# Kernel optimization log

Measured on AMD Instinct MI355X. Metric: run time of the kernel, lower is better.

Reference implementation:

```python
import jax, jax.numpy as jnp
import numpy as np

B, N, DIM = 4, 2048, 256
K = 16            # num_nearest_neighbors
EDGE_DIM = 2
M_DIM = 64
EIN = 2 * DIM + 1 + EDGE_DIM   # 515, edge_mlp input dim
VALID_RADIUS = 0.0
MASK_FILL = 1e5


def setup_inputs() -> dict:
    key = jax.random.key(0)
    ks = jax.random.split(key, 16)
    emb = jax.random.normal(ks[0], (B, N, DIM), dtype=jnp.float32)
    coors = jax.random.normal(ks[1], (B, N, 3), dtype=jnp.float32)
    adj = jax.random.bernoulli(ks[2], 0.004, (B, N, N))            # avg degree ~8
    feat = jax.random.normal(ks[3], (B, N, N, EDGE_DIM), dtype=jnp.float32)
    mask = jax.random.bernoulli(ks[4], 0.9, (B, N))
    s = 0.02
    eW1 = jax.random.normal(ks[5], (EIN, 2 * EIN), dtype=jnp.float32) * s
    eb1 = jnp.zeros((2 * EIN,), dtype=jnp.float32)
    eW2 = jax.random.normal(ks[6], (2 * EIN, M_DIM), dtype=jnp.float32) * s
    eb2 = jnp.zeros((M_DIM,), dtype=jnp.float32)
    nW1 = jax.random.normal(ks[7], (DIM + M_DIM, 2 * DIM), dtype=jnp.float32) * s
    nb1 = jnp.zeros((2 * DIM,), dtype=jnp.float32)
    nW2 = jax.random.normal(ks[8], (2 * DIM, DIM), dtype=jnp.float32) * s
    nb2 = jnp.zeros((DIM,), dtype=jnp.float32)
    return {"emb": emb, "coors": coors, "adj": adj, "feat": feat, "mask": mask,
            "eW1": eW1, "eb1": eb1, "eW2": eW2, "eb2": eb2,
            "nW1": nW1, "nb1": nb1, "nW2": nW2, "nb2": nb2}


def reference(emb, coors, adj, feat, mask, eW1, eb1, eW2, eb2, nW1, nb1, nW2, nb2):
    b, n, d = emb.shape
    # pairwise squared distances [b,n,n]
    rel = coors[:, :, None, :] - coors[:, None, :, :]
    rel_dist = jnp.sum(rel * rel, axis=-1)
    # ranking for kNN selection (masked pairs pushed far, self=-1, adjacent=0)
    rank_mask = mask[:, :, None] & mask[:, None, :]
    ranking = jnp.where(rank_mask, rel_dist, MASK_FILL)
    eye = jnp.eye(n, dtype=bool)[None]
    adj_ns = adj & ~eye
    ranking = jnp.where(eye, -1.0, ranking)
    ranking = jnp.where(adj_ns, 0.0, ranking)
    # k smallest
    neg_vals, idx = jax.lax.top_k(-ranking, K)          # idx [b,n,K]
    nbhd_ranking = -neg_vals
    nbhd_mask = nbhd_ranking <= VALID_RADIUS
    # gathers
    rel_dist_k = jnp.take_along_axis(rel_dist, idx, axis=2)[..., None]      # [b,n,K,1]
    edges_k = jnp.take_along_axis(feat, idx[..., None], axis=2)             # [b,n,K,E]
    feats_j = jax.vmap(lambda f, ix: f[ix])(emb, idx)                       # [b,n,K,d]
    feats_i = jnp.broadcast_to(emb[:, :, None, :], feats_j.shape)
    edge_input = jnp.concatenate([feats_i, feats_j, rel_dist_k, edges_k], axis=-1)
    # edge MLP: Linear -> SiLU -> Linear -> SiLU (dropout=0 in eval)
    h = jax.nn.silu(edge_input @ eW1 + eb1)
    m_ij = jax.nn.silu(h @ eW2 + eb2)                                       # [b,n,K,m]
    # pair mask
    mask_j = jax.vmap(lambda m, ix: m[ix])(mask, idx)                       # [b,n,K]
    pair_mask = (mask[:, :, None] & mask_j) & nbhd_mask
    m_ij = jnp.where(pair_mask[..., None], m_ij, 0.0)
    m_i = jnp.sum(m_ij, axis=2)                                             # [b,n,m]
    # node MLP with residual (norm_feats=False)
    node_in = jnp.concatenate([emb, m_i], axis=-1)
    node_out = jax.nn.silu(node_in @ nW1 + nb1) @ nW2 + nb2 + emb
    # update_coors=False -> coors unchanged; module returns full tuple
    return (node_out, coors, adj, feat, mask)
```

## Files before the change

### kernel.cpp

```cpp
#include <hip/hip_runtime.h>
#include <stdint.h>

typedef unsigned short ushort_t;

#define NN    2048
#define DIMC  256
#define H1    1030
#define MD    64
#define NROWS 8192

#define HP       1040

#define KPAD     1152
#define CH       288
#define CH_STEPS 9
#define NCHUNK   4
#define APAD     296
#define GPC      36

#define NPQ      2060
#define NPQP     2112
#define KN1      320
#define KN2      512

typedef __bf16 bf16x8 __attribute__((ext_vector_type(8)));
typedef float  f32x4  __attribute__((ext_vector_type(4)));
typedef float  f32x2  __attribute__((ext_vector_type(2)));
typedef ushort_t u16x8 __attribute__((ext_vector_type(8)));

__device__ __forceinline__ float bfu2f(ushort_t u){ union{unsigned u; float f;} v; v.u = ((unsigned)u)<<16; return v.f; }
__device__ __forceinline__ ushort_t f2bfu(float f){ union{float f; unsigned u;} v; v.f=f; unsigned r = (v.u + 0x7FFFu + ((v.u>>16)&1u))>>16; return (ushort_t)r; }
__device__ __forceinline__ float siluf(float x){ return x / (1.0f + __expf(-x)); }
__device__ __forceinline__ void split_hilo(float v, ushort_t& hi, ushort_t& lo){
    hi = f2bfu(v);
    lo = f2bfu(v - bfu2f(hi));
}

__global__ void mask_kernel(const int* __restrict__ mask, float* __restrict__ out_mask){
    int t = blockIdx.x*256 + threadIdx.x;
    if (t < NROWS) out_mask[t] = mask[t] ? 1.0f : 0.0f;
}

__global__ void adj_kernel(const int* __restrict__ adj, const int* __restrict__ mask,
                           float* __restrict__ out_adj, int* __restrict__ pairs,
                           int* __restrict__ counter)
{
    const int w = threadIdx.x >> 6, lane = threadIdx.x & 63;
    const int row = blockIdx.x*4 + w;
    const int b = row >> 11, i = row & (NN-1);
    __shared__ int nbrs[4][15];
    int total = 0;
    const size_t rbase = (size_t)row * NN;
    for (int c = 0; c < NN/64; c++) {
        int j = c*64 + lane;
        int v = adj[rbase + j];
        out_adj[rbase + j] = v ? 1.0f : 0.0f;
        bool pred = (v != 0) && (j != i);
        unsigned long long bm = __ballot(pred);
        if (pred) {
            int slot = total + __popcll(bm & ((1ull<<lane)-1ull));
            if (slot < 15) nbrs[w][slot] = j;
        }
        total += __popcll(bm);
    }
    int cnt = total < 15 ? total : 15;
    if (mask[row] != 0) {
        int jl = (lane < cnt) ? nbrs[w][lane] : 0;
        bool ok = (lane < cnt) && (mask[b*NN + jl] != 0);
        unsigned long long bm = __ballot(ok);
        int npair = 1 + __popcll(bm);
        int basep = 0;
        if (lane == 0) basep = atomicAdd(counter, npair);
        basep = __shfl(basep, 0);
        if (lane == 0) pairs[basep] = (row << 16) | i;
        if (ok) {
            int pos = basep + 1 + __popcll(bm & ((1ull<<lane)-1ull));
            pairs[pos] = (row << 16) | jl;
        }
    }
}

template<int K>
__device__ __forceinline__ void mfma_tile2(const ushort_t* __restrict__ Ah, const ushort_t* __restrict__ Al, int sA,
                                           const ushort_t* __restrict__ Bh, const ushort_t* __restrict__ Bl, int sB,
                                           int lane, f32x4 (&acc)[2][4])
{
    const int m16 = lane & 15, kg = lane >> 4;
    const ushort_t* a0h = Ah + (size_t)m16*sA + kg*8;
    const ushort_t* a0l = Al + (size_t)m16*sA + kg*8;
    const ushort_t* a1h = a0h + (size_t)16*sA;
    const ushort_t* a1l = a0l + (size_t)16*sA;
    const ushort_t* brh = Bh + (size_t)m16*sB + kg*8;
    const ushort_t* brl = Bl + (size_t)m16*sB + kg*8;
#pragma unroll 4
    for (int ks = 0; ks < K/32; ks++) {
        bf16x8 a0h_ = *reinterpret_cast<const bf16x8*>(a0h + ks*32);
        bf16x8 a0l_ = *reinterpret_cast<const bf16x8*>(a0l + ks*32);
        bf16x8 a1h_ = *reinterpret_cast<const bf16x8*>(a1h + ks*32);
        bf16x8 a1l_ = *reinterpret_cast<const bf16x8*>(a1l + ks*32);
#pragma unroll
        for (int nf = 0; nf < 4; nf++) {
            bf16x8 bh = *reinterpret_cast<const bf16x8*>(brh + (size_t)(nf*16)*sB + ks*32);
            bf16x8 bl = *reinterpret_cast<const bf16x8*>(brl + (size_t)(nf*16)*sB + ks*32);
            acc[0][nf] = __builtin_amdgcn_mfma_f32_16x16x32_bf16(a0h_, bh, acc[0][nf], 0, 0, 0);
            acc[0][nf] = __builtin_amdgcn_mfma_f32_16x16x32_bf16(a0h_, bl, acc[0][nf], 0, 0, 0);
            acc[0][nf] = __builtin_amdgcn_mfma_f32_16x16x32_bf16(a0l_, bh, acc[0][nf], 0, 0, 0);
            acc[1][nf] = __builtin_amdgcn_mfma_f32_16x16x32_bf16(a1h_, bh, acc[1][nf], 0, 0, 0);
            acc[1][nf] = __builtin_amdgcn_mfma_f32_16x16x32_bf16(a1h_, bl, acc[1][nf], 0, 0, 0);
            acc[1][nf] = __builtin_amdgcn_mfma_f32_16x16x32_bf16(a1l_, bh, acc[1][nf], 0, 0, 0);
        }
    }
}

__global__ void prep_emb(const float* __restrict__ emb, ushort_t* __restrict__ Ah, ushort_t* __restrict__ Al){
    int t = blockIdx.x*256 + threadIdx.x;
    if (t >= NROWS*DIMC) return;
    int r = t >> 8, k = t & 255;
    ushort_t hi, lo; split_hilo(emb[t], hi, lo);
    Ah[(size_t)r*KN1 + k] = hi; Al[(size_t)r*KN1 + k] = lo;
}

__global__ void prep_macc(const float* __restrict__ macc, ushort_t* __restrict__ Ah, ushort_t* __restrict__ Al){
    int t = blockIdx.x*256 + threadIdx.x;
    if (t >= NROWS*MD) return;
    int r = t >> 6, k = t & 63;
    ushort_t hi, lo; split_hilo(macc[t], hi, lo);
    Ah[(size_t)r*KN1 + DIMC + k] = hi; Al[(size_t)r*KN1 + DIMC + k] = lo;
}

__global__ void prep_weights(const float* __restrict__ eW1, const float* __restrict__ nW1,
                             const float* __restrict__ nW2, const float* __restrict__ eW2,
                             const float* __restrict__ eb1,
                             ushort_t* __restrict__ Wpq_h, ushort_t* __restrict__ Wpq_l,
                             ushort_t* __restrict__ W1T_h, ushort_t* __restrict__ W1T_l,
                             ushort_t* __restrict__ NW2T_h, ushort_t* __restrict__ NW2T_l,
                             ushort_t* __restrict__ W2T, float* __restrict__ wt4)
{
    int t = blockIdx.x*256 + threadIdx.x;
    if (t < NPQP*DIMC) {
        int n = t >> 8, k = t & 255;
        float v = 0.f;
        if (n < H1) v = eW1[(size_t)k*H1 + n];
        else if (n < NPQ) v = eW1[(size_t)(256+k)*H1 + (n - H1)];
        ushort_t hi, lo; split_hilo(v, hi, lo);
        Wpq_h[t] = hi; Wpq_l[t] = lo;
        return;
    }
    t -= NPQP*DIMC;
    if (t < 512*KN1) {
        int n = t / KN1, k = t - n*KN1;
        ushort_t hi, lo; split_hilo(nW1[(size_t)k*512 + n], hi, lo);
        W1T_h[t] = hi; W1T_l[t] = lo;
        return;
    }
    t -= 512*KN1;
    if (t < 256*KN2) {
        int n = t >> 9, k = t & 511;
        ushort_t hi, lo; split_hilo(nW2[(size_t)k*256 + n], hi, lo);
        NW2T_h[t] = hi; NW2T_l[t] = lo;
        return;
    }
    t -= 256*KN2;
    if (t < MD*KPAD) {
        int n = t / KPAD, k = t - n*KPAD;
        W2T[t] = f2bfu((k < H1) ? eW2[(size_t)k*MD + n] : 0.0f);
        return;
    }
    t -= MD*KPAD;
    if (t < 4*HP) {
        int c = t / HP, k = t - c*HP;
        float v = 0.f;
        if (k < H1) v = (c < 3) ? eW1[(size_t)(512+c)*H1 + k] : eb1[k];
        wt4[t] = v;
    }
}

__global__ __launch_bounds__(256)
void gemm_pq_mfma(const ushort_t* __restrict__ Aeph, const ushort_t* __restrict__ Aepl,
                  const ushort_t* __restrict__ Wh, const ushort_t* __restrict__ Wl,
                  ushort_t* __restrict__ Pb, ushort_t* __restrict__ Qb)
{
    const int lane = threadIdx.x & 63, w = threadIdx.x >> 6;
    const int rowBase = blockIdx.x*128 + w*32;
    const int colBase = blockIdx.y*64;
    f32x4 acc[2][4] = {{{0,0,0,0},{0,0,0,0},{0,0,0,0},{0,0,0,0}},
                       {{0,0,0,0},{0,0,0,0},{0,0,0,0},{0,0,0,0}}};
    mfma_tile2<DIMC>(Aeph + (size_t)rowBase*KN1, Aepl + (size_t)rowBase*KN1, KN1,
                     Wh + (size_t)colBase*DIMC, Wl + (size_t)colBase*DIMC, DIMC, lane, acc);
    const int m16 = lane & 15, kg = lane >> 4;
#pragma unroll
    for (int tt = 0; tt < 2; tt++) {
#pragma unroll
        for (int nf = 0; nf < 4; nf++) {
#pragma unroll
            for (int r = 0; r < 4; r++) {
                int row = rowBase + tt*16 + kg*4 + r;
                int n = colBase + nf*16 + m16;
                ushort_t v = f2bfu(acc[tt][nf][r]);
                if (n < H1)        Pb[(size_t)row*HP + n] = v;
                else if (n < NPQ)  Qb[(size_t)row*HP + (n - H1)] = v;
            }
        }
    }
}

__global__ __launch_bounds__(256)
void node1_mfma(const ushort_t* __restrict__ Aeph, const ushort_t* __restrict__ Aepl,
                const ushort_t* __restrict__ W1h, const ushort_t* __restrict__ W1l,
                const float* __restrict__ nb1, ushort_t* __restrict__ Hh, ushort_t* __restrict__ Hl)
{
    const int lane = threadIdx.x & 63, w = threadIdx.x >> 6;
    const int rowBase = blockIdx.x*128 + w*32;
    const int colBase = blockIdx.y*64;
    f32x4 acc[2][4] = {{{0,0,0,0},{0,0,0,0},{0,0,0,0},{0,0,0,0}},
                       {{0,0,0,0},{0,0,0,0},{0,0,0,0},{0,0,0,0}}};
    mfma_tile2<KN1>(Aeph + (size_t)rowBase*KN1, Aepl + (size_t)rowBase*KN1, KN1,
                    W1h + (size_t)colBase*KN1, W1l + (size_t)colBase*KN1, KN1, lane, acc);
    const int m16 = lane & 15, kg = lane >> 4;
#pragma unroll
    for (int tt = 0; tt < 2; tt++) {
#pragma unroll
        for (int nf = 0; nf < 4; nf++) {
#pragma unroll
            for (int r = 0; r < 4; r++) {
                int row = rowBase + tt*16 + kg*4 + r;
                int col = colBase + nf*16 + m16;
                float s = siluf(acc[tt][nf][r] + nb1[col]);
                ushort_t hi, lo; split_hilo(s, hi, lo);
                Hh[(size_t)row*KN2 + col] = hi;
                Hl[(size_t)row*KN2 + col] = lo;
            }
        }
    }
}

__global__ __launch_bounds__(256)
void node2_mfma(const ushort_t* __restrict__ Hh, const ushort_t* __restrict__ Hl,
                const ushort_t* __restrict__ W2h, const ushort_t* __restrict__ W2l,
                const float* __restrict__ nb2, const float* __restrict__ emb,
                float* __restrict__ out_node)
{
    const int lane = threadIdx.x & 63, w = threadIdx.x >> 6;
    const int rowBase = blockIdx.x*128 + w*32;
    const int colBase = blockIdx.y*64;
    f32x4 acc[2][4] = {{{0,0,0,0},{0,0,0,0},{0,0,0,0},{0,0,0,0}},
                       {{0,0,0,0},{0,0,0,0},{0,0,0,0},{0,0,0,0}}};
    mfma_tile2<KN2>(Hh + (size_t)rowBase*KN2, Hl + (size_t)rowBase*KN2, KN2,
                    W2h + (size_t)colBase*KN2, W2l + (size_t)colBase*KN2, KN2, lane, acc);
    const int m16 = lane & 15, kg = lane >> 4;
#pragma unroll
    for (int tt = 0; tt < 2; tt++) {
#pragma unroll
        for (int nf = 0; nf < 4; nf++) {
#pragma unroll
            for (int r = 0; r < 4; r++) {
                int row = rowBase + tt*16 + kg*4 + r;
                int col = colBase + nf*16 + m16;
                size_t o = (size_t)row*DIMC + col;
                out_node[o] = acc[tt][nf][r] + nb2[col] + emb[o];
            }
        }
    }
}

__global__ __launch_bounds__(256)
void edge_mfma(const int* __restrict__ pairs, const int* __restrict__ counter,
               const ushort_t* __restrict__ P, const ushort_t* __restrict__ Q,
               const float* __restrict__ coors, const float* __restrict__ feat,
               const float* __restrict__ wt4,
               const ushort_t* __restrict__ W2T, const float* __restrict__ eb2,
               float* __restrict__ macc)
{
    const int np = counter[0];
    const int base = blockIdx.x * 16;
    if (base >= np) return;

    __shared__ __align__(16) ushort_t Ahi[16][APAD];
    __shared__ __align__(16) ushort_t Alo[16][APAD];
    __shared__ int   s_row[16];
    __shared__ int   s_jr[16];
    __shared__ int   s_val[16];
    __shared__ float s_d[16], s_f0[16], s_f1[16];

    const int t = threadIdx.x;
    const int lane = t & 63;
    const int w = t >> 6;

    if (t < 16) {
        int ip = base + t;
        int valid = (ip < np) ? 1 : 0;
        int e = valid ? pairs[ip] : 0;
        int row = e >> 16, j = e & 0xFFFF;
        int jr = ((row >> 11) << 11) + j;
        float dx = coors[(size_t)row*3+0] - coors[(size_t)jr*3+0];
        float dy = coors[(size_t)row*3+1] - coors[(size_t)jr*3+1];
        float dz = coors[(size_t)row*3+2] - coors[(size_t)jr*3+2];
        size_t fo = ((size_t)row*NN + j)*2;
        s_row[t] = row; s_jr[t] = jr; s_val[t] = valid;
        s_d[t] = dx*dx + dy*dy + dz*dz;
        s_f0[t] = feat[fo]; s_f1[t] = feat[fo+1];
    }
    __syncthreads();

    const int pp  = lane >> 4;
    const int sub = lane & 15;
    const int p   = w*4 + pp;
    const int prow = s_row[p], pjr = s_jr[p];
    const float pd = s_d[p], pf0 = s_f0[p], pf1 = s_f1[p];
    const ushort_t* Prow = P + (size_t)prow*HP;
    const ushort_t* Qrow = Q + (size_t)pjr*HP;

    const float* w512 = wt4 + 0*HP;
    const float* w513 = wt4 + 1*HP;
    const float* w514 = wt4 + 2*HP;
    const float* bia1 = wt4 + 3*HP;

    f32x4 acc = {0.f, 0.f, 0.f, 0.f};

    const int m16  = lane & 15;
    const int kg   = lane >> 4;
    const int ncol = w*16 + m16;
    const ushort_t* wrowbase = W2T + (size_t)ncol * KPAD + kg*8;

    for (int chunk = 0; chunk < NCHUNK; chunk++) {
        const int c0 = chunk * CH;
#pragma unroll
        for (int it = 0; it < 3; it++) {
            int g = sub + it*16;
            if (g < GPC) {
                int cb  = g*8;
                int ccb = c0 + cb;
                u16x8 hv = {0,0,0,0,0,0,0,0};
                u16x8 lv = {0,0,0,0,0,0,0,0};
                if (ccb < H1) {
                    u16x8 pv8 = *reinterpret_cast<const u16x8*>(Prow + ccb);
                    u16x8 qv8 = *reinterpret_cast<const u16x8*>(Qrow + ccb);
                    f32x2 wa[4], wb[4], wc[4], wd[4];
#pragma unroll
                    for (int q = 0; q < 4; q++) {
                        wa[q] = *reinterpret_cast<const f32x2*>(w512 + ccb + q*2);
                        wb[q] = *reinterpret_cast<const f32x2*>(w513 + ccb + q*2);
                        wc[q] = *reinterpret_cast<const f32x2*>(w514 + ccb + q*2);
                        wd[q] = *reinterpret_cast<const f32x2*>(bia1 + ccb + q*2);
                    }
#pragma unroll
                    for (int e = 0; e < 8; e++) {
                        float x = bfu2f(pv8[e]) + bfu2f(qv8[e])
                                + pd*wa[e>>1][e&1] + pf0*wb[e>>1][e&1] + pf1*wc[e>>1][e&1] + wd[e>>1][e&1];
                        float h = (ccb + e < H1) ? siluf(x) : 0.f;
                        union {float f; unsigned u;} cv; cv.f = h;
                        unsigned hib = cv.u & 0xFFFF0000u;
                        hv[e] = (ushort_t)(hib >> 16);
                        union {unsigned u; float f;} hf; hf.u = hib;
                        union {float f; unsigned u;} lw; lw.f = h - hf.f;
                        lv[e] = (ushort_t)(lw.u >> 16);
                    }
                }
                *reinterpret_cast<u16x8*>(&Ahi[p][cb]) = hv;
                *reinterpret_cast<u16x8*>(&Alo[p][cb]) = lv;
            }
        }
        __syncthreads();
        const ushort_t* wrow = wrowbase + c0;
#pragma unroll
        for (int ks = 0; ks < CH_STEPS; ks++) {
            int k = ks*32 + kg*8;
            bf16x8 ahi = *reinterpret_cast<const bf16x8*>(&Ahi[m16][k]);
            bf16x8 alo = *reinterpret_cast<const bf16x8*>(&Alo[m16][k]);
            bf16x8 bfr = *reinterpret_cast<const bf16x8*>(wrow + ks*32);
            acc = __builtin_amdgcn_mfma_f32_16x16x32_bf16(ahi, bfr, acc, 0, 0, 0);
            acc = __builtin_amdgcn_mfma_f32_16x16x32_bf16(alo, bfr, acc, 0, 0, 0);
        }
        __syncthreads();
    }

    {
        float bias = eb2[ncol];
#pragma unroll
        for (int r = 0; r < 4; r++) {
            int pe = kg*4 + r;
            if (s_val[pe]) {
                float m = siluf(acc[r] + bias);
                atomicAdd(&macc[(size_t)s_row[pe]*MD + ncol], m);
            }
        }
    }
}

extern "C" void kernel_launch(void* const* d_in, const int* in_sizes, int n_in,
                              void* d_out, int out_size, void* d_ws, size_t ws_size,
                              hipStream_t stream)
{
    const float* emb   = (const float*)d_in[0];
    const float* coors = (const float*)d_in[1];
    const int*   adj   = (const int*)d_in[2];
    const float* feat  = (const float*)d_in[3];
    const int*   mask  = (const int*)d_in[4];
    const float* eW1   = (const float*)d_in[5];
    const float* eb1   = (const float*)d_in[6];
    const float* eW2   = (const float*)d_in[7];
    const float* eb2   = (const float*)d_in[8];
    const float* nW1   = (const float*)d_in[9];
    const float* nb1   = (const float*)d_in[10];
    const float* nW2   = (const float*)d_in[11];
    const float* nb2   = (const float*)d_in[12];

    float* out       = (float*)d_out;
    float* out_node  = out;
    float* out_coors = out + 2097152;
    float* out_adj   = out + 2121728;
    float* out_feat  = out + 18898944;
    float* out_mask  = out + 52453376;

    char* ws = (char*)d_ws;
    int*      counter = (int*)(ws + 0);
    float*    macc    = (float*)(ws + 256);
    int*      pairs   = (int*)(ws + 2097408);
    ushort_t* Pbuf    = (ushort_t*)(ws + 2621696);
    float*    wt4     = (float*)(ws + 19661056);

    char* scr = (char*)out_feat;
    ushort_t* Aep_h = (ushort_t*)(scr + 0);
    ushort_t* Aep_l = (ushort_t*)(scr + 5242880);
    ushort_t* Wpq_h = (ushort_t*)(scr + 10485760);
    ushort_t* Wpq_l = (ushort_t*)(scr + 11567104);
    ushort_t* W1T_h = (ushort_t*)(scr + 12648448);
    ushort_t* W1T_l = (ushort_t*)(scr + 12976128);
    ushort_t* NW2T_h= (ushort_t*)(scr + 13303808);
    ushort_t* NW2T_l= (ushort_t*)(scr + 13565952);
    ushort_t* Hid_h = (ushort_t*)(scr + 13828096);
    ushort_t* Hid_l = (ushort_t*)(scr + 22216704);
    ushort_t* Qbuf  = (ushort_t*)(scr + 30605312);

    ushort_t* W2T = (ushort_t*)out_node;

    hipMemsetAsync(counter, 0, 256, stream);
    hipMemsetAsync(macc, 0, (size_t)NROWS*MD*sizeof(float), stream);

    hipMemcpyAsync(out_coors, coors, (size_t)24576*sizeof(float), hipMemcpyDeviceToDevice, stream);

    mask_kernel<<<(NROWS + 255)/256, 256, 0, stream>>>(mask, out_mask);
    adj_kernel<<<NROWS/4, 256, 0, stream>>>(adj, mask, out_adj, pairs, counter);

    prep_emb<<<(NROWS*DIMC + 255)/256, 256, 0, stream>>>(emb, Aep_h, Aep_l);
    {
        int tot = NPQP*DIMC + 512*KN1 + 256*KN2 + MD*KPAD + 4*HP;
        prep_weights<<<(tot + 255)/256, 256, 0, stream>>>(eW1, nW1, nW2, eW2, eb1,
                                                          Wpq_h, Wpq_l, W1T_h, W1T_l,
                                                          NW2T_h, NW2T_l, W2T, wt4);
    }

    gemm_pq_mfma<<<dim3(NROWS/128, NPQP/64), 256, 0, stream>>>(Aep_h, Aep_l, Wpq_h, Wpq_l, Pbuf, Qbuf);

    edge_mfma<<<NROWS*16/16, 256, 0, stream>>>(pairs, counter, Pbuf, Qbuf, coors, feat,
                                               wt4, W2T, eb2, macc);

    prep_macc<<<(NROWS*MD + 255)/256, 256, 0, stream>>>(macc, Aep_h, Aep_l);
    node1_mfma<<<dim3(NROWS/128, 512/64), 256, 0, stream>>>(Aep_h, Aep_l, W1T_h, W1T_l, nb1, Hid_h, Hid_l);
    node2_mfma<<<dim3(NROWS/128, DIMC/64), 256, 0, stream>>>(Hid_h, Hid_l, NW2T_h, NW2T_l, nb2, emb, out_node);

    hipMemcpyAsync(out_feat, feat, (size_t)33554432*sizeof(float), hipMemcpyDeviceToDevice, stream);
}
```

Baseline: 770.3 us.

## Restructure edge kernel per-wave, fold bias into PQ GEMM, merge prep kernels

The edge MLP kernel now gives each wave its own 16 pairs with the hidden activations kept in registers, so the shared-memory staging and block barriers are gone and each wave computes all 64 output columns. The first-layer bias eb1 is added in the PQ GEMM epilogue instead of per edge. The mask conversion is folded into the adjacency kernel, which now reads int4 vectors, and the emb hi/lo split is merged into prep_weights. This cuts kernel launches and synchronisation, but each wave now reloads W2T rows from global memory and does more atomics per wave.

```diff
diff --git a/kernel.cpp b/kernel.cpp
--- a/kernel.cpp
+++ b/kernel.cpp
@@ -11,12 +11,8 @@
 
 #define HP       1040
 
-#define KPAD     1152
-#define CH       288
-#define CH_STEPS 9
-#define NCHUNK   4
-#define APAD     296
-#define GPC      36
+#define KPAD     1056
+#define NKS      33
 
 #define NPQ      2060
 #define NPQP     2112
@@ -25,7 +21,6 @@
 
 typedef __bf16 bf16x8 __attribute__((ext_vector_type(8)));
 typedef float  f32x4  __attribute__((ext_vector_type(4)));
-typedef float  f32x2  __attribute__((ext_vector_type(2)));
 typedef ushort_t u16x8 __attribute__((ext_vector_type(8)));
 
 __device__ __forceinline__ float bfu2f(ushort_t u){ union{unsigned u; float f;} v; v.u = ((unsigned)u)<<16; return v.f; }
@@ -36,14 +31,9 @@
     lo = f2bfu(v - bfu2f(hi));
 }
 
-__global__ void mask_kernel(const int* __restrict__ mask, float* __restrict__ out_mask){
-    int t = blockIdx.x*256 + threadIdx.x;
-    if (t < NROWS) out_mask[t] = mask[t] ? 1.0f : 0.0f;
-}
-
 __global__ void adj_kernel(const int* __restrict__ adj, const int* __restrict__ mask,
-                           float* __restrict__ out_adj, int* __restrict__ pairs,
-                           int* __restrict__ counter)
+                           float* __restrict__ out_adj, float* __restrict__ out_mask,
+                           int* __restrict__ pairs, int* __restrict__ counter)
 {
     const int w = threadIdx.x >> 6, lane = threadIdx.x & 63;
     const int row = blockIdx.x*4 + w;
@@ -51,20 +41,33 @@
     __shared__ int nbrs[4][15];
     int total = 0;
     const size_t rbase = (size_t)row * NN;
-    for (int c = 0; c < NN/64; c++) {
-        int j = c*64 + lane;
-        int v = adj[rbase + j];
-        out_adj[rbase + j] = v ? 1.0f : 0.0f;
-        bool pred = (v != 0) && (j != i);
-        unsigned long long bm = __ballot(pred);
-        if (pred) {
-            int slot = total + __popcll(bm & ((1ull<<lane)-1ull));
-            if (slot < 15) nbrs[w][slot] = j;
-        }
-        total += __popcll(bm);
+    const int4* arow = (const int4*)(adj + rbase);
+    float4* orow = (float4*)(out_adj + rbase);
+    for (int c = 0; c < NN/256; c++) {
+        int4 v = arow[c*64 + lane];
+        int j0 = c*256 + lane*4;
+        float4 ov; ov.x = v.x?1.f:0.f; ov.y = v.y?1.f:0.f; ov.z = v.z?1.f:0.f; ov.w = v.w?1.f:0.f;
+        orow[c*64 + lane] = ov;
+        bool p0 = v.x && (j0   != i);
+        bool p1 = v.y && (j0+1 != i);
+        bool p2 = v.z && (j0+2 != i);
+        bool p3 = v.w && (j0+3 != i);
+        unsigned long long b0 = __ballot(p0), b1 = __ballot(p1), b2 = __ballot(p2), b3 = __ballot(p3);
+        unsigned long long below = (1ull<<lane)-1ull;
+        int slot = total + __popcll(b0&below)+__popcll(b1&below)+__popcll(b2&below)+__popcll(b3&below);
+        if (p0 && slot < 15) nbrs[w][slot] = j0;
+        slot += p0;
+        if (p1 && slot < 15) nbrs[w][slot] = j0+1;
+        slot += p1;
+        if (p2 && slot < 15) nbrs[w][slot] = j0+2;
+        slot += p2;
+        if (p3 && slot < 15) nbrs[w][slot] = j0+3;
+        total += __popcll(b0)+__popcll(b1)+__popcll(b2)+__popcll(b3);
     }
     int cnt = total < 15 ? total : 15;
-    if (mask[row] != 0) {
+    const int mv = mask[row];
+    if (lane == 0) out_mask[row] = mv ? 1.0f : 0.0f;
+    if (mv != 0) {
         int jl = (lane < cnt) ? nbrs[w][lane] : 0;
         bool ok = (lane < cnt) && (mask[b*NN + jl] != 0);
         unsigned long long bm = __ballot(ok);
@@ -112,29 +115,14 @@
     }
 }
 
-__global__ void prep_emb(const float* __restrict__ emb, ushort_t* __restrict__ Ah, ushort_t* __restrict__ Al){
-    int t = blockIdx.x*256 + threadIdx.x;
-    if (t >= NROWS*DIMC) return;
-    int r = t >> 8, k = t & 255;
-    ushort_t hi, lo; split_hilo(emb[t], hi, lo);
-    Ah[(size_t)r*KN1 + k] = hi; Al[(size_t)r*KN1 + k] = lo;
-}
-
-__global__ void prep_macc(const float* __restrict__ macc, ushort_t* __restrict__ Ah, ushort_t* __restrict__ Al){
-    int t = blockIdx.x*256 + threadIdx.x;
-    if (t >= NROWS*MD) return;
-    int r = t >> 6, k = t & 63;
-    ushort_t hi, lo; split_hilo(macc[t], hi, lo);
-    Ah[(size_t)r*KN1 + DIMC + k] = hi; Al[(size_t)r*KN1 + DIMC + k] = lo;
-}
-
 __global__ void prep_weights(const float* __restrict__ eW1, const float* __restrict__ nW1,
                              const float* __restrict__ nW2, const float* __restrict__ eW2,
-                             const float* __restrict__ eb1,
+                             const float* __restrict__ emb,
                              ushort_t* __restrict__ Wpq_h, ushort_t* __restrict__ Wpq_l,
                              ushort_t* __restrict__ W1T_h, ushort_t* __restrict__ W1T_l,
                              ushort_t* __restrict__ NW2T_h, ushort_t* __restrict__ NW2T_l,
-                             ushort_t* __restrict__ W2T, float* __restrict__ wt4)
+                             ushort_t* __restrict__ W2T, float* __restrict__ wt4,
+                             ushort_t* __restrict__ Ah, ushort_t* __restrict__ Al)
 {
     int t = blockIdx.x*256 + threadIdx.x;
     if (t < NPQP*DIMC) {
@@ -167,17 +155,31 @@
         return;
     }
     t -= MD*KPAD;
-    if (t < 4*HP) {
+    if (t < 3*HP) {
         int c = t / HP, k = t - c*HP;
-        float v = 0.f;
-        if (k < H1) v = (c < 3) ? eW1[(size_t)(512+c)*H1 + k] : eb1[k];
-        wt4[t] = v;
-    }
+        wt4[t] = (k < H1) ? eW1[(size_t)(512+c)*H1 + k] : 0.f;
+        return;
+    }
+    t -= 3*HP;
+    if (t < NROWS*DIMC) {
+        int r = t >> 8, k = t & 255;
+        ushort_t hi, lo; split_hilo(emb[t], hi, lo);
+        Ah[(size_t)r*KN1 + k] = hi; Al[(size_t)r*KN1 + k] = lo;
+    }
+}
+
+__global__ void prep_macc(const float* __restrict__ macc, ushort_t* __restrict__ Ah, ushort_t* __restrict__ Al){
+    int t = blockIdx.x*256 + threadIdx.x;
+    if (t >= NROWS*MD) return;
+    int r = t >> 6, k = t & 63;
+    ushort_t hi, lo; split_hilo(macc[t], hi, lo);
+    Ah[(size_t)r*KN1 + DIMC + k] = hi; Al[(size_t)r*KN1 + DIMC + k] = lo;
 }
 
 __global__ __launch_bounds__(256)
 void gemm_pq_mfma(const ushort_t* __restrict__ Aeph, const ushort_t* __restrict__ Aepl,
                   const ushort_t* __restrict__ Wh, const ushort_t* __restrict__ Wl,
+                  const float* __restrict__ eb1,
                   ushort_t* __restrict__ Pb, ushort_t* __restrict__ Qb)
 {
     const int lane = threadIdx.x & 63, w = threadIdx.x >> 6;
@@ -196,9 +198,11 @@
             for (int r = 0; r < 4; r++) {
                 int row = rowBase + tt*16 + kg*4 + r;
                 int n = colBase + nf*16 + m16;
-                ushort_t v = f2bfu(acc[tt][nf][r]);
-                if (n < H1)        Pb[(size_t)row*HP + n] = v;
-                else if (n < NPQ)  Qb[(size_t)row*HP + (n - H1)] = v;
+                if (n < H1) {
+                    Pb[(size_t)row*HP + n] = f2bfu(acc[tt][nf][r] + eb1[n]);
+                } else if (n < NPQ) {
+                    Qb[(size_t)row*HP + (n - H1)] = f2bfu(acc[tt][nf][r]);
+                }
             }
         }
     }
@@ -272,116 +276,81 @@
                float* __restrict__ macc)
 {
     const int np = counter[0];
-    const int base = blockIdx.x * 16;
-    if (base >= np) return;
-
-    __shared__ __align__(16) ushort_t Ahi[16][APAD];
-    __shared__ __align__(16) ushort_t Alo[16][APAD];
-    __shared__ int   s_row[16];
-    __shared__ int   s_jr[16];
-    __shared__ int   s_val[16];
-    __shared__ float s_d[16], s_f0[16], s_f1[16];
-
-    const int t = threadIdx.x;
-    const int lane = t & 63;
-    const int w = t >> 6;
-
-    if (t < 16) {
-        int ip = base + t;
-        int valid = (ip < np) ? 1 : 0;
-        int e = valid ? pairs[ip] : 0;
-        int row = e >> 16, j = e & 0xFFFF;
-        int jr = ((row >> 11) << 11) + j;
-        float dx = coors[(size_t)row*3+0] - coors[(size_t)jr*3+0];
-        float dy = coors[(size_t)row*3+1] - coors[(size_t)jr*3+1];
-        float dz = coors[(size_t)row*3+2] - coors[(size_t)jr*3+2];
-        size_t fo = ((size_t)row*NN + j)*2;
-        s_row[t] = row; s_jr[t] = jr; s_val[t] = valid;
-        s_d[t] = dx*dx + dy*dy + dz*dz;
-        s_f0[t] = feat[fo]; s_f1[t] = feat[fo+1];
-    }
-    __syncthreads();
-
-    const int pp  = lane >> 4;
-    const int sub = lane & 15;
-    const int p   = w*4 + pp;
-    const int prow = s_row[p], pjr = s_jr[p];
-    const float pd = s_d[p], pf0 = s_f0[p], pf1 = s_f1[p];
-    const ushort_t* Prow = P + (size_t)prow*HP;
-    const ushort_t* Qrow = Q + (size_t)pjr*HP;
-
-    const float* w512 = wt4 + 0*HP;
-    const float* w513 = wt4 + 1*HP;
+    const int lane = threadIdx.x & 63;
+    const int w = threadIdx.x >> 6;
+    const int wbase = blockIdx.x*64 + w*16;
+    if (wbase >= np) return;
+    const int m16 = lane & 15, kg = lane >> 4;
+
+    const int pidx = wbase + m16;
+    const int e = pairs[(pidx < np) ? pidx : wbase];
+    const int row = e >> 16, j = e & 0xFFFF;
+    const int jr = ((row >> 11) << 11) + j;
+    const float dx = coors[row*3+0] - coors[jr*3+0];
+    const float dy = coors[row*3+1] - coors[jr*3+1];
+    const float dz = coors[row*3+2] - coors[jr*3+2];
+    const float d  = dx*dx + dy*dy + dz*dz;
+    const size_t fo = ((size_t)row*NN + j)*2;
+    const float f0 = feat[fo], f1 = feat[fo+1];
+    const ushort_t* Prow = P + (size_t)row*HP;
+    const ushort_t* Qrow = Q + (size_t)jr*HP;
+    const float* w512 = wt4;
+    const float* w513 = wt4 + HP;
     const float* w514 = wt4 + 2*HP;
-    const float* bia1 = wt4 + 3*HP;
-
-    f32x4 acc = {0.f, 0.f, 0.f, 0.f};
-
-    const int m16  = lane & 15;
-    const int kg   = lane >> 4;
-    const int ncol = w*16 + m16;
-    const ushort_t* wrowbase = W2T + (size_t)ncol * KPAD + kg*8;
-
-    for (int chunk = 0; chunk < NCHUNK; chunk++) {
-        const int c0 = chunk * CH;
-#pragma unroll
-        for (int it = 0; it < 3; it++) {
-            int g = sub + it*16;
-            if (g < GPC) {
-                int cb  = g*8;
-                int ccb = c0 + cb;
-                u16x8 hv = {0,0,0,0,0,0,0,0};
-                u16x8 lv = {0,0,0,0,0,0,0,0};
-                if (ccb < H1) {
-                    u16x8 pv8 = *reinterpret_cast<const u16x8*>(Prow + ccb);
-                    u16x8 qv8 = *reinterpret_cast<const u16x8*>(Qrow + ccb);
-                    f32x2 wa[4], wb[4], wc[4], wd[4];
-#pragma unroll
-                    for (int q = 0; q < 4; q++) {
-                        wa[q] = *reinterpret_cast<const f32x2*>(w512 + ccb + q*2);
-                        wb[q] = *reinterpret_cast<const f32x2*>(w513 + ccb + q*2);
-                        wc[q] = *reinterpret_cast<const f32x2*>(w514 + ccb + q*2);
-                        wd[q] = *reinterpret_cast<const f32x2*>(bia1 + ccb + q*2);
-                    }
-#pragma unroll
-                    for (int e = 0; e < 8; e++) {
-                        float x = bfu2f(pv8[e]) + bfu2f(qv8[e])
-                                + pd*wa[e>>1][e&1] + pf0*wb[e>>1][e&1] + pf1*wc[e>>1][e&1] + wd[e>>1][e&1];
-                        float h = (ccb + e < H1) ? siluf(x) : 0.f;
-                        union {float f; unsigned u;} cv; cv.f = h;
-                        unsigned hib = cv.u & 0xFFFF0000u;
-                        hv[e] = (ushort_t)(hib >> 16);
-                        union {unsigned u; float f;} hf; hf.u = hib;
-                        union {float f; unsigned u;} lw; lw.f = h - hf.f;
-                        lv[e] = (ushort_t)(lw.u >> 16);
-                    }
-                }
-                *reinterpret_cast<u16x8*>(&Ahi[p][cb]) = hv;
-                *reinterpret_cast<u16x8*>(&Alo[p][cb]) = lv;
+    const int kb = kg*8;
+
+    f32x4 acc[4] = {{0,0,0,0},{0,0,0,0},{0,0,0,0},{0,0,0,0}};
+
+    for (int ks = 0; ks < NKS; ks++) {
+        const int k0 = ks*32 + kb;
+        u16x8 hv = {0,0,0,0,0,0,0,0};
+        u16x8 lv = {0,0,0,0,0,0,0,0};
+        if (k0 < H1) {
+            u16x8 pv8 = *reinterpret_cast<const u16x8*>(Prow + k0);
+            u16x8 qv8 = *reinterpret_cast<const u16x8*>(Qrow + k0);
+            f32x4 wa0 = *reinterpret_cast<const f32x4*>(w512 + k0);
+            f32x4 wa1 = *reinterpret_cast<const f32x4*>(w512 + k0 + 4);
+            f32x4 wb0 = *reinterpret_cast<const f32x4*>(w513 + k0);
+            f32x4 wb1 = *reinterpret_cast<const f32x4*>(w513 + k0 + 4);
+            f32x4 wc0 = *reinterpret_cast<const f32x4*>(w514 + k0);
+            f32x4 wc1 = *reinterpret_cast<const f32x4*>(w514 + k0 + 4);
+#pragma unroll
+            for (int ee = 0; ee < 8; ee++) {
+                float va = (ee < 4) ? wa0[ee] : wa1[ee-4];
+                float vb = (ee < 4) ? wb0[ee] : wb1[ee-4];
+                float vc = (ee < 4) ? wc0[ee] : wc1[ee-4];
+                float x = bfu2f(pv8[ee]) + bfu2f(qv8[ee]) + d*va + f0*vb + f1*vc;
+                float h = (k0 + ee < H1) ? siluf(x) : 0.f;
+                union {float f; unsigned u;} cv; cv.f = h;
+                unsigned hib = cv.u & 0xFFFF0000u;
+                hv[ee] = (ushort_t)(hib >> 16);
+                union {unsigned u; float f;} hf; hf.u = hib;
+                union {float f; unsigned u;} lw; lw.f = h - hf.f;
+                lv[ee] = (ushort_t)(lw.u >> 16);
             }
         }
-        __syncthreads();
-        const ushort_t* wrow = wrowbase + c0;
-#pragma unroll
-        for (int ks = 0; ks < CH_STEPS; ks++) {
-            int k = ks*32 + kg*8;
-            bf16x8 ahi = *reinterpret_cast<const bf16x8*>(&Ahi[m16][k]);
-            bf16x8 alo = *reinterpret_cast<const bf16x8*>(&Alo[m16][k]);
-            bf16x8 bfr = *reinterpret_cast<const bf16x8*>(wrow + ks*32);
-            acc = __builtin_amdgcn_mfma_f32_16x16x32_bf16(ahi, bfr, acc, 0, 0, 0);
-            acc = __builtin_amdgcn_mfma_f32_16x16x32_bf16(alo, bfr, acc, 0, 0, 0);
-        }
-        __syncthreads();
-    }
-
-    {
-        float bias = eb2[ncol];
+        bf16x8 ah = *reinterpret_cast<bf16x8*>(&hv);
+        bf16x8 al = *reinterpret_cast<bf16x8*>(&lv);
+        const ushort_t* Wk = W2T + k0;
+#pragma unroll
+        for (int nf = 0; nf < 4; nf++) {
+            bf16x8 bfr = *reinterpret_cast<const bf16x8*>(Wk + (size_t)(nf*16 + m16)*KPAD);
+            acc[nf] = __builtin_amdgcn_mfma_f32_16x16x32_bf16(ah, bfr, acc[nf], 0, 0, 0);
+            acc[nf] = __builtin_amdgcn_mfma_f32_16x16x32_bf16(al, bfr, acc[nf], 0, 0, 0);
+        }
+    }
+
+#pragma unroll
+    for (int nf = 0; nf < 4; nf++) {
+        const int n = nf*16 + m16;
+        const float bias = eb2[n];
 #pragma unroll
         for (int r = 0; r < 4; r++) {
-            int pe = kg*4 + r;
-            if (s_val[pe]) {
-                float m = siluf(acc[r] + bias);
-                atomicAdd(&macc[(size_t)s_row[pe]*MD + ncol], m);
+            int pe = wbase + kg*4 + r;
+            if (pe < np) {
+                int rr = pairs[pe] >> 16;
+                float m = siluf(acc[nf][r] + bias);
+                atomicAdd(&macc[(size_t)rr*MD + n], m);
             }
         }
     }
@@ -439,21 +408,20 @@
 
     hipMemcpyAsync(out_coors, coors, (size_t)24576*sizeof(float), hipMemcpyDeviceToDevice, stream);
 
-    mask_kernel<<<(NROWS + 255)/256, 256, 0, stream>>>(mask, out_mask);
-    adj_kernel<<<NROWS/4, 256, 0, stream>>>(adj, mask, out_adj, pairs, counter);
-
-    prep_emb<<<(NROWS*DIMC + 255)/256, 256, 0, stream>>>(emb, Aep_h, Aep_l);
+    adj_kernel<<<NROWS/4, 256, 0, stream>>>(adj, mask, out_adj, out_mask, pairs, counter);
+
     {
-        int tot = NPQP*DIMC + 512*KN1 + 256*KN2 + MD*KPAD + 4*HP;
-        prep_weights<<<(tot + 255)/256, 256, 0, stream>>>(eW1, nW1, nW2, eW2, eb1,
+        int tot = NPQP*DIMC + 512*KN1 + 256*KN2 + MD*KPAD + 3*HP + NROWS*DIMC;
+        prep_weights<<<(tot + 255)/256, 256, 0, stream>>>(eW1, nW1, nW2, eW2, emb,
                                                           Wpq_h, Wpq_l, W1T_h, W1T_l,
-                                                          NW2T_h, NW2T_l, W2T, wt4);
-    }
-
-    gemm_pq_mfma<<<dim3(NROWS/128, NPQP/64), 256, 0, stream>>>(Aep_h, Aep_l, Wpq_h, Wpq_l, Pbuf, Qbuf);
-
-    edge_mfma<<<NROWS*16/16, 256, 0, stream>>>(pairs, counter, Pbuf, Qbuf, coors, feat,
-                                               wt4, W2T, eb2, macc);
+                                                          NW2T_h, NW2T_l, W2T, wt4,
+                                                          Aep_h, Aep_l);
+    }
+
+    gemm_pq_mfma<<<dim3(NROWS/128, NPQP/64), 256, 0, stream>>>(Aep_h, Aep_l, Wpq_h, Wpq_l, eb1, Pbuf, Qbuf);
+
+    edge_mfma<<<2048, 256, 0, stream>>>(pairs, counter, Pbuf, Qbuf, coors, feat,
+                                        wt4, W2T, eb2, macc);
 
     prep_macc<<<(NROWS*MD + 255)/256, 256, 0, stream>>>(macc, Aep_h, Aep_l);
     node1_mfma<<<dim3(NROWS/128, 512/64), 256, 0, stream>>>(Aep_h, Aep_l, W1T_h, W1T_l, nb1, Hid_h, Hid_l);
```

Result: faster. 725.1 us (-5.9%).
